# Optimization experiments

Measured on AMD Instinct MI355X. Metric: run time of the kernel, lower is better.

## Reference

```python
import jax, jax.numpy as jnp
import numpy as np
from jax import lax

NUM_VOCAB = 16384
DIM_EMBED = 4
LOSS_COEFF = 0.25


def setup_inputs() -> dict:
    key = jax.random.key(0)
    k1, k2 = jax.random.split(key)
    x = jax.random.normal(k1, (8, DIM_EMBED, 32, 32), dtype=jnp.float32)
    # nn.Embedding weight initialized uniform(-1/K, 1/K)
    lim = 1.0 / NUM_VOCAB
    codebook = jax.random.uniform(k2, (NUM_VOCAB, DIM_EMBED), dtype=jnp.float32,
                                  minval=-lim, maxval=lim)
    return {"x": x, "codebook": codebook}


def reference(x, codebook):
    # x: [B, C, H, W] -> [B, H, W, C]
    z = jnp.transpose(x, (0, 2, 3, 1))
    B, H, W, C = z.shape
    zf = z.reshape(-1, C)  # [N, C]
    # squared distances ||z||^2 + ||e||^2 - 2 z.e  -> [N, K]
    d = (jnp.sum(zf * zf, axis=1, keepdims=True)
         + jnp.sum(codebook * codebook, axis=1)
         - 2.0 * jnp.matmul(zf, codebook.T))
    idx = jnp.argmin(d, axis=1)  # [N]
    embed = codebook[idx].reshape(z.shape)  # [B, H, W, C]
    loss = (jnp.mean((lax.stop_gradient(embed) - z) ** 2)
            + LOSS_COEFF * jnp.mean((embed - lax.stop_gradient(z)) ** 2))
    # straight-through estimator
    embed_st = z + lax.stop_gradient(embed - z)
    out = jnp.transpose(embed_st, (0, 3, 1, 2))  # [B, C, H, W]
    return out, loss, idx
```

## Files before the change

### kernel.cpp

```cpp
#include <hip/hip_runtime.h>


#define NUM_VOCAB 16384
#define NROWS 8192
#define NELEM 32768
#define CODES_PER_WAVE 256
#define ROWS_PER_LANE 4


__global__ __launch_bounds__(256) void k_init(const float* __restrict__ cb,
                                              float* __restrict__ ee,
                                              unsigned long long* __restrict__ packed,
                                              double* __restrict__ accum) {
    int i = blockIdx.x * 256 + threadIdx.x;
    if (i < NUM_VOCAB) {
        float e0 = cb[i * 4 + 0], e1 = cb[i * 4 + 1];
        float e2 = cb[i * 4 + 2], e3 = cb[i * 4 + 3];
        float s = __fadd_rn(__fadd_rn(__fadd_rn(__fmul_rn(e0, e0),
                                                __fmul_rn(e1, e1)),
                                      __fmul_rn(e2, e2)),
                            __fmul_rn(e3, e3));
        ee[i] = s;
    }
    if (i < NROWS) packed[i] = 0xFFFFFFFFFFFFFFFFULL;
    if (i == 0) *accum = 0.0;
}

__global__ __launch_bounds__(256) void k_argmin(const float* __restrict__ x,
                                                const float* __restrict__ cb,
                                                const float* __restrict__ ee,
                                                unsigned long long* __restrict__ packed) {
    const int lane = threadIdx.x & 63;
    const int wave = __builtin_amdgcn_readfirstlane(threadIdx.x >> 6);
    const int tile = blockIdx.x;
    const int cg   = blockIdx.y;
    const int k0   = (cg * 4 + wave) * CODES_PER_WAVE;

    float z0[ROWS_PER_LANE], z1[ROWS_PER_LANE], z2[ROWS_PER_LANE], z3[ROWS_PER_LANE];
    float zz[ROWS_PER_LANE];
#pragma unroll
    for (int r = 0; r < ROWS_PER_LANE; ++r) {
        const int row = tile * 256 + r * 64 + lane;
        const int b = row >> 10, p = row & 1023;
        const float* xb = x + b * 4096 + p;
        z0[r] = xb[0]; z1[r] = xb[1024]; z2[r] = xb[2048]; z3[r] = xb[3072];
        zz[r] = __fadd_rn(__fadd_rn(__fadd_rn(__fmul_rn(z0[r], z0[r]),
                                              __fmul_rn(z1[r], z1[r])),
                                    __fmul_rn(z2[r], z2[r])),
                          __fmul_rn(z3[r], z3[r]));
    }

    float best[ROWS_PER_LANE];
    int   bk[ROWS_PER_LANE];
#pragma unroll
    for (int r = 0; r < ROWS_PER_LANE; ++r) { best[r] = 3.4e38f; bk[r] = 0; }

    const float4* cb4 = (const float4*)cb;
#pragma unroll 8
    for (int kk = 0; kk < CODES_PER_WAVE; ++kk) {
        const int k = k0 + kk;
        const float4 e  = cb4[k];
        const float eek = ee[k];
#pragma unroll
        for (int r = 0; r < ROWS_PER_LANE; ++r) {
            float dot = __builtin_fmaf(z3[r], e.w,
                        __builtin_fmaf(z2[r], e.z,
                        __builtin_fmaf(z1[r], e.y, __fmul_rn(z0[r], e.x))));
            float t = __fadd_rn(zz[r], eek);
            float d = __builtin_fmaf(-2.0f, dot, t);
            if (d < best[r]) { best[r] = d; bk[r] = k; }
        }
    }

#pragma unroll
    for (int r = 0; r < ROWS_PER_LANE; ++r) {
        const int row = tile * 256 + r * 64 + lane;
        unsigned long long key =
            ((unsigned long long)__float_as_uint(best[r]) << 32) | (unsigned)bk[r];
        atomicMin(&packed[row], key);
    }
}

__global__ __launch_bounds__(256) void k_final(const float* __restrict__ x,
                                               const float* __restrict__ cb,
                                               const unsigned long long* __restrict__ packed,
                                               float* __restrict__ out,
                                               double* __restrict__ accum) {
    const int n = blockIdx.x * 256 + threadIdx.x;
    const int b = n >> 10, p = n & 1023;
    const float* xb = x + b * 4096 + p;
    const float z0 = xb[0], z1 = xb[1024], z2 = xb[2048], z3 = xb[3072];

    const int k = (int)(unsigned)(packed[n] & 0xFFFFFFFFULL);
    const float e0 = cb[k * 4 + 0], e1 = cb[k * 4 + 1];
    const float e2 = cb[k * 4 + 2], e3 = cb[k * 4 + 3];

    float* ob = out + b * 4096 + p;
    ob[0] = e0; ob[1024] = e1; ob[2048] = e2; ob[3072] = e3;
    out[NELEM + 1 + n] = (float)k;

    const float d0 = e0 - z0, d1 = e1 - z1, d2 = e2 - z2, d3 = e3 - z3;
    double v = (double)d0 * d0 + (double)d1 * d1 + (double)d2 * d2 + (double)d3 * d3;

    for (int o = 32; o > 0; o >>= 1) v += __shfl_down(v, o);
    __shared__ double sred[4];
    if ((threadIdx.x & 63) == 0) sred[threadIdx.x >> 6] = v;
    __syncthreads();
    if (threadIdx.x == 0) {
        double t = sred[0] + sred[1] + sred[2] + sred[3];
        atomicAdd(accum, t);
    }
}

__global__ void k_loss(const double* __restrict__ accum, float* __restrict__ out) {
    float m = (float)(*accum / (double)NELEM);
    out[NELEM] = m + 0.25f * m;
}

extern "C" void kernel_launch(void* const* d_in, const int* in_sizes, int n_in,
                              void* d_out, int out_size, void* d_ws, size_t ws_size,
                              hipStream_t stream) {
    const float* x  = (const float*)d_in[0];
    const float* cb = (const float*)d_in[1];
    float* out = (float*)d_out;

    char* w = (char*)d_ws;
    float* ee = (float*)w;
    unsigned long long* packed = (unsigned long long*)(w + 65536);
    double* accum = (double*)(w + 131072);

    k_init<<<dim3(NUM_VOCAB / 256), dim3(256), 0, stream>>>(cb, ee, packed, accum);
    k_argmin<<<dim3(NROWS / 256, NUM_VOCAB / (4 * CODES_PER_WAVE)), dim3(256), 0, stream>>>(
        x, cb, ee, packed);
    k_final<<<dim3(NROWS / 256), dim3(256), 0, stream>>>(x, cb, packed, out, accum);
    k_loss<<<dim3(1), dim3(1), 0, stream>>>(accum, out);
}
```

Measured before the change: 101.1 us.

## Fuse init into argmin, replace atomics with per-group slots, fold loss into final

The separate init and loss kernels are removed, cutting the launch count from four to two. Each argmin block now computes codebook norms into LDS and reduces its 8 waves in shared memory. It writes per-codegroup minima to slot buffers instead of issuing 64-bit atomicMin calls. The final kernel reduces the 16 slots per row and uses a last-block counter to write the loss. A fallback path keeps the old four-kernel scheme when the workspace is too small; it adds a larger workspace need and redundant norm computation per block.

Measured after the change: 89.42 us. 1.13x faster.

```diff
diff --git a/kernel.cpp b/kernel.cpp
--- a/kernel.cpp
+++ b/kernel.cpp
@@ -4,37 +4,39 @@
 #define NUM_VOCAB 16384
 #define NROWS 8192
 #define NELEM 32768
-#define CODES_PER_WAVE 256
+#define NCG 16
+#define CODES_PER_BLOCK 1024
+#define CODES_PER_WAVE 128
 #define ROWS_PER_LANE 4
 
-
-__global__ __launch_bounds__(256) void k_init(const float* __restrict__ cb,
-                                              float* __restrict__ ee,
-                                              unsigned long long* __restrict__ packed,
-                                              double* __restrict__ accum) {
-    int i = blockIdx.x * 256 + threadIdx.x;
-    if (i < NUM_VOCAB) {
-        float e0 = cb[i * 4 + 0], e1 = cb[i * 4 + 1];
-        float e2 = cb[i * 4 + 2], e3 = cb[i * 4 + 3];
-        float s = __fadd_rn(__fadd_rn(__fadd_rn(__fmul_rn(e0, e0),
-                                                __fmul_rn(e1, e1)),
-                                      __fmul_rn(e2, e2)),
-                            __fmul_rn(e3, e3));
-        ee[i] = s;
-    }
-    if (i < NROWS) packed[i] = 0xFFFFFFFFFFFFFFFFULL;
-    if (i == 0) *accum = 0.0;
-}
-
-__global__ __launch_bounds__(256) void k_argmin(const float* __restrict__ x,
-                                                const float* __restrict__ cb,
-                                                const float* __restrict__ ee,
-                                                unsigned long long* __restrict__ packed) {
-    const int lane = threadIdx.x & 63;
-    const int wave = __builtin_amdgcn_readfirstlane(threadIdx.x >> 6);
+#define SLOT_BYTES (NCG * NROWS * 8)
+#define WS_MAIN_BYTES (SLOT_BYTES + 16)
+
+__global__ __launch_bounds__(512, 4) void k_argmin(const float* __restrict__ x,
+                                                   const float* __restrict__ cb,
+                                                   unsigned long long* __restrict__ slots,
+                                                   double* __restrict__ accum,
+                                                   unsigned int* __restrict__ counter) {
+    const int tid  = threadIdx.x;
+    const int lane = tid & 63;
+    const int wave = __builtin_amdgcn_readfirstlane(tid >> 6);
     const int tile = blockIdx.x;
     const int cg   = blockIdx.y;
-    const int k0   = (cg * 4 + wave) * CODES_PER_WAVE;
+
+    if (tile == 0 && cg == 0 && tid == 0) { *accum = 0.0; *counter = 0u; }
+
+    __shared__ float eeLDS[CODES_PER_BLOCK];
+    __shared__ unsigned long long red[8][256];
+
+    const float4* cb4 = (const float4*)cb;
+
+    for (int l = tid; l < CODES_PER_BLOCK; l += 512) {
+        const float4 e = cb4[cg * CODES_PER_BLOCK + l];
+        eeLDS[l] = __fadd_rn(__fadd_rn(__fadd_rn(__fmul_rn(e.x, e.x),
+                                                 __fmul_rn(e.y, e.y)),
+                                       __fmul_rn(e.z, e.z)),
+                             __fmul_rn(e.w, e.w));
+    }
 
     float z0[ROWS_PER_LANE], z1[ROWS_PER_LANE], z2[ROWS_PER_LANE], z3[ROWS_PER_LANE];
     float zz[ROWS_PER_LANE];
@@ -49,18 +51,20 @@
                                     __fmul_rn(z2[r], z2[r])),
                           __fmul_rn(z3[r], z3[r]));
     }
+    __syncthreads();
 
     float best[ROWS_PER_LANE];
     int   bk[ROWS_PER_LANE];
 #pragma unroll
     for (int r = 0; r < ROWS_PER_LANE; ++r) { best[r] = 3.4e38f; bk[r] = 0; }
 
-    const float4* cb4 = (const float4*)cb;
+    const int k0 = cg * CODES_PER_BLOCK + wave * CODES_PER_WAVE;
+    const int l0 = wave * CODES_PER_WAVE;
 #pragma unroll 8
     for (int kk = 0; kk < CODES_PER_WAVE; ++kk) {
         const int k = k0 + kk;
         const float4 e  = cb4[k];
-        const float eek = ee[k];
+        const float eek = eeLDS[l0 + kk];
 #pragma unroll
         for (int r = 0; r < ROWS_PER_LANE; ++r) {
             float dot = __builtin_fmaf(z3[r], e.w,
@@ -74,6 +78,128 @@
 
 #pragma unroll
     for (int r = 0; r < ROWS_PER_LANE; ++r) {
+        red[wave][r * 64 + lane] =
+            ((unsigned long long)__float_as_uint(best[r]) << 32) | (unsigned)bk[r];
+    }
+    __syncthreads();
+
+    if (tid < 256) {
+        unsigned long long m = red[0][tid];
+#pragma unroll
+        for (int w2 = 1; w2 < 8; ++w2) {
+            unsigned long long s = red[w2][tid];
+            if (s < m) m = s;
+        }
+        slots[cg * NROWS + tile * 256 + tid] = m;
+    }
+}
+
+__global__ __launch_bounds__(256) void k_final(const float* __restrict__ x,
+                                               const float* __restrict__ cb,
+                                               const unsigned long long* __restrict__ slots,
+                                               float* __restrict__ out,
+                                               double* __restrict__ accum,
+                                               unsigned int* __restrict__ counter) {
+    const int n = blockIdx.x * 256 + threadIdx.x;
+
+    unsigned long long m = slots[n];
+#pragma unroll
+    for (int cg = 1; cg < NCG; ++cg) {
+        unsigned long long s = slots[cg * NROWS + n];
+        if (s < m) m = s;
+    }
+    const int k = (int)(unsigned)(m & 0xFFFFFFFFULL);
+
+    const int b = n >> 10, p = n & 1023;
+    const float* xb = x + b * 4096 + p;
+    const float z0 = xb[0], z1 = xb[1024], z2 = xb[2048], z3 = xb[3072];
+    const float e0 = cb[k * 4 + 0], e1 = cb[k * 4 + 1];
+    const float e2 = cb[k * 4 + 2], e3 = cb[k * 4 + 3];
+
+    float* ob = out + b * 4096 + p;
+    ob[0] = e0; ob[1024] = e1; ob[2048] = e2; ob[3072] = e3;
+    out[NELEM + 1 + n] = (float)k;
+
+    const float d0 = e0 - z0, d1 = e1 - z1, d2 = e2 - z2, d3 = e3 - z3;
+    double v = (double)d0 * d0 + (double)d1 * d1 + (double)d2 * d2 + (double)d3 * d3;
+
+    for (int o = 32; o > 0; o >>= 1) v += __shfl_down(v, o);
+    __shared__ double sred[4];
+    if ((threadIdx.x & 63) == 0) sred[threadIdx.x >> 6] = v;
+    __syncthreads();
+    if (threadIdx.x == 0) {
+        atomicAdd(accum, sred[0] + sred[1] + sred[2] + sred[3]);
+        __threadfence();
+        unsigned int prev = atomicAdd(counter, 1u);
+        if (prev == (NROWS / 256) - 1) {
+            __threadfence();
+            double tot = atomicAdd(accum, 0.0);
+            float mloss = (float)(tot / (double)NELEM);
+            out[NELEM] = mloss + 0.25f * mloss;
+        }
+    }
+}
+
+
+__global__ __launch_bounds__(256) void fb_init(const float* __restrict__ cb,
+                                               float* __restrict__ ee,
+                                               unsigned long long* __restrict__ packed,
+                                               double* __restrict__ accum) {
+    int i = blockIdx.x * 256 + threadIdx.x;
+    if (i < NUM_VOCAB) {
+        float e0 = cb[i * 4 + 0], e1 = cb[i * 4 + 1];
+        float e2 = cb[i * 4 + 2], e3 = cb[i * 4 + 3];
+        ee[i] = __fadd_rn(__fadd_rn(__fadd_rn(__fmul_rn(e0, e0),
+                                              __fmul_rn(e1, e1)),
+                                    __fmul_rn(e2, e2)),
+                          __fmul_rn(e3, e3));
+    }
+    if (i < NROWS) packed[i] = 0xFFFFFFFFFFFFFFFFULL;
+    if (i == 0) *accum = 0.0;
+}
+
+__global__ __launch_bounds__(256) void fb_argmin(const float* __restrict__ x,
+                                                 const float* __restrict__ cb,
+                                                 const float* __restrict__ ee,
+                                                 unsigned long long* __restrict__ packed) {
+    const int lane = threadIdx.x & 63;
+    const int wave = __builtin_amdgcn_readfirstlane(threadIdx.x >> 6);
+    const int tile = blockIdx.x, cg = blockIdx.y;
+    const int k0 = (cg * 4 + wave) * 256;
+
+    float z0[4], z1[4], z2[4], z3[4], zz[4];
+#pragma unroll
+    for (int r = 0; r < 4; ++r) {
+        const int row = tile * 256 + r * 64 + lane;
+        const int b = row >> 10, p = row & 1023;
+        const float* xb = x + b * 4096 + p;
+        z0[r] = xb[0]; z1[r] = xb[1024]; z2[r] = xb[2048]; z3[r] = xb[3072];
+        zz[r] = __fadd_rn(__fadd_rn(__fadd_rn(__fmul_rn(z0[r], z0[r]),
+                                              __fmul_rn(z1[r], z1[r])),
+                                    __fmul_rn(z2[r], z2[r])),
+                          __fmul_rn(z3[r], z3[r]));
+    }
+    float best[4]; int bk[4];
+#pragma unroll
+    for (int r = 0; r < 4; ++r) { best[r] = 3.4e38f; bk[r] = 0; }
+    const float4* cb4 = (const float4*)cb;
+#pragma unroll 8
+    for (int kk = 0; kk < 256; ++kk) {
+        const int k = k0 + kk;
+        const float4 e = cb4[k];
+        const float eek = ee[k];
+#pragma unroll
+        for (int r = 0; r < 4; ++r) {
+            float dot = __builtin_fmaf(z3[r], e.w,
+                        __builtin_fmaf(z2[r], e.z,
+                        __builtin_fmaf(z1[r], e.y, __fmul_rn(z0[r], e.x))));
+            float t = __fadd_rn(zz[r], eek);
+            float d = __builtin_fmaf(-2.0f, dot, t);
+            if (d < best[r]) { best[r] = d; bk[r] = k; }
+        }
+    }
+#pragma unroll
+    for (int r = 0; r < 4; ++r) {
         const int row = tile * 256 + r * 64 + lane;
         unsigned long long key =
             ((unsigned long long)__float_as_uint(best[r]) << 32) | (unsigned)bk[r];
@@ -81,38 +207,31 @@
     }
 }
 
-__global__ __launch_bounds__(256) void k_final(const float* __restrict__ x,
-                                               const float* __restrict__ cb,
-                                               const unsigned long long* __restrict__ packed,
-                                               float* __restrict__ out,
-                                               double* __restrict__ accum) {
+__global__ __launch_bounds__(256) void fb_final(const float* __restrict__ x,
+                                                const float* __restrict__ cb,
+                                                const unsigned long long* __restrict__ packed,
+                                                float* __restrict__ out,
+                                                double* __restrict__ accum) {
     const int n = blockIdx.x * 256 + threadIdx.x;
     const int b = n >> 10, p = n & 1023;
     const float* xb = x + b * 4096 + p;
     const float z0 = xb[0], z1 = xb[1024], z2 = xb[2048], z3 = xb[3072];
-
     const int k = (int)(unsigned)(packed[n] & 0xFFFFFFFFULL);
     const float e0 = cb[k * 4 + 0], e1 = cb[k * 4 + 1];
     const float e2 = cb[k * 4 + 2], e3 = cb[k * 4 + 3];
-
     float* ob = out + b * 4096 + p;
     ob[0] = e0; ob[1024] = e1; ob[2048] = e2; ob[3072] = e3;
     out[NELEM + 1 + n] = (float)k;
-
     const float d0 = e0 - z0, d1 = e1 - z1, d2 = e2 - z2, d3 = e3 - z3;
     double v = (double)d0 * d0 + (double)d1 * d1 + (double)d2 * d2 + (double)d3 * d3;
-
     for (int o = 32; o > 0; o >>= 1) v += __shfl_down(v, o);
     __shared__ double sred[4];
     if ((threadIdx.x & 63) == 0) sred[threadIdx.x >> 6] = v;
     __syncthreads();
-    if (threadIdx.x == 0) {
-        double t = sred[0] + sred[1] + sred[2] + sred[3];
-        atomicAdd(accum, t);
-    }
-}
-
-__global__ void k_loss(const double* __restrict__ accum, float* __restrict__ out) {
+    if (threadIdx.x == 0) atomicAdd(accum, sred[0] + sred[1] + sred[2] + sred[3]);
+}
+
+__global__ void fb_loss(const double* __restrict__ accum, float* __restrict__ out) {
     float m = (float)(*accum / (double)NELEM);
     out[NELEM] = m + 0.25f * m;
 }
@@ -123,15 +242,24 @@
     const float* x  = (const float*)d_in[0];
     const float* cb = (const float*)d_in[1];
     float* out = (float*)d_out;
-
     char* w = (char*)d_ws;
-    float* ee = (float*)w;
-    unsigned long long* packed = (unsigned long long*)(w + 65536);
-    double* accum = (double*)(w + 131072);
-
-    k_init<<<dim3(NUM_VOCAB / 256), dim3(256), 0, stream>>>(cb, ee, packed, accum);
-    k_argmin<<<dim3(NROWS / 256, NUM_VOCAB / (4 * CODES_PER_WAVE)), dim3(256), 0, stream>>>(
-        x, cb, ee, packed);
-    k_final<<<dim3(NROWS / 256), dim3(256), 0, stream>>>(x, cb, packed, out, accum);
-    k_loss<<<dim3(1), dim3(1), 0, stream>>>(accum, out);
-}
+
+    if (ws_size >= (size_t)WS_MAIN_BYTES) {
+        unsigned long long* slots = (unsigned long long*)w;
+        double* accum = (double*)(w + SLOT_BYTES);
+        unsigned int* counter = (unsigned int*)(w + SLOT_BYTES + 8);
+        k_argmin<<<dim3(NROWS / 256, NCG), dim3(512), 0, stream>>>(
+            x, cb, slots, accum, counter);
+        k_final<<<dim3(NROWS / 256), dim3(256), 0, stream>>>(
+            x, cb, slots, out, accum, counter);
+    } else {
+        float* ee = (float*)w;
+        unsigned long long* packed = (unsigned long long*)(w + 65536);
+        double* accum = (double*)(w + 131072);
+        fb_init<<<dim3(NUM_VOCAB / 256), dim3(256), 0, stream>>>(cb, ee, packed, accum);
+        fb_argmin<<<dim3(NROWS / 256, NUM_VOCAB / 1024), dim3(256), 0, stream>>>(
+            x, cb, ee, packed);
+        fb_final<<<dim3(NROWS / 256), dim3(256), 0, stream>>>(x, cb, packed, out, accum);
+        fb_loss<<<dim3(1), dim3(1), 0, stream>>>(accum, out);
+    }
+}
```
